# Optimization experiments

Measured on AMD Instinct MI355X. Metric: run time of the kernel, lower is better.

## Reference

```python
import jax, jax.numpy as jnp
import numpy as np

B, CIN, COUT, K, H, W, WDIM = 16, 512, 512, 3, 64, 64, 512


def setup_inputs() -> dict:
    key = jax.random.key(0)
    k1, k2, k3, k4 = jax.random.split(key, 4)
    x = jax.random.normal(k1, (B, CIN, H, W), dtype=jnp.float32)
    w = jax.random.normal(k2, (B, WDIM), dtype=jnp.float32)
    # Equalized-LR init: init_std = 1/lrmul = 1.0 -> unit normal weights
    conv_w = jax.random.normal(k3, (K, K, CIN, COUT), dtype=jnp.float32)
    mod_w = jax.random.normal(k4, (WDIM, CIN), dtype=jnp.float32)
    mod_b = jnp.zeros((CIN,), dtype=jnp.float32)
    return {"x": x, "w": w, "conv_w": conv_w, "mod_w": mod_w, "mod_b": mod_b}


def reference(x, w, conv_w, mod_w, mod_b):
    # runtime coefficients (gain=1, lrmul=1): he_std = gain/sqrt(fan_in)
    coef_conv = np.float32(1.0 / np.sqrt(K * K * CIN))
    coef_mod = np.float32(1.0 / np.sqrt(WDIM))

    # style modulation: Dense + Bias + 1.0  -> [B, CIN]
    style = w @ (coef_mod * mod_w) + mod_b + 1.0

    # per-sample modulated weight [B, K, K, CIN, COUT]
    weight = (coef_conv * conv_w)[None] * style[:, None, None, :, None]

    # demodulate: rsqrt of sum of squares over (K, K, CIN) per output channel
    d = jax.lax.rsqrt(jnp.sum(jnp.square(weight), axis=(1, 2, 3)) + 1e-8)  # [B, COUT]
    weight = weight * d[:, None, None, None, :]

    # grouped conv via batch->channel-group reshape (StyleGAN2 trick)
    wg = jnp.transpose(weight, (1, 2, 3, 0, 4)).reshape(K, K, CIN, B * COUT)
    xg = x.reshape(1, B * CIN, H, W)
    y = jax.lax.conv_general_dilated(
        xg, wg, window_strides=(1, 1), padding="SAME",
        dimension_numbers=("NCHW", "HWIO", "NCHW"),
        feature_group_count=B,
    )
    return y.reshape(B, COUT, H, W)
```

## Files before the change

### kernel.cpp

```cpp
#include <hip/hip_runtime.h>
#include <hip/hip_bf16.h>

#define NB    16
#define CIN   512
#define COUT  512
#define HH    64
#define WW    64
#define HWSZ  4096
#define WDIMN 512

typedef __attribute__((ext_vector_type(8))) short bf16x8;
typedef __attribute__((ext_vector_type(4))) float f32x4;

__device__ __forceinline__ unsigned short f2bf(float f) {
    unsigned int u = __float_as_uint(f);
    unsigned int lsb = (u >> 16) & 1u;
    u += 0x7fffu + lsb;
    return (unsigned short)(u >> 16);
}

__device__ __forceinline__ void gload_lds16(const void* g, void* l) {
    __builtin_amdgcn_global_load_lds(
        (const __attribute__((address_space(1))) unsigned char*)g,
        (__attribute__((address_space(3))) unsigned char*)l,
        16, 0, 0);
}

__global__ void k_style(const float* __restrict__ w, const float* __restrict__ mod_w,
                        const float* __restrict__ mod_b, float* __restrict__ style) {
    const int b = blockIdx.x, t = threadIdx.x;
    __shared__ float wl[WDIMN];
    wl[t] = w[b * WDIMN + t];
    wl[t + 256] = w[b * WDIMN + t + 256];
    __syncthreads();
    float a0 = 0.f, a1 = 0.f;
    const int c0 = t, c1 = t + 256;
    for (int j = 0; j < WDIMN; ++j) {
        const float wj = wl[j];
        a0 += wj * mod_w[j * CIN + c0];
        a1 += wj * mod_w[j * CIN + c1];
    }
    const float coef = 0.044194173824159216f;
    style[b * CIN + c0] = coef * a0 + mod_b[c0] + 1.0f;
    style[b * CIN + c1] = coef * a1 + mod_b[c1] + 1.0f;
}

__global__ void k_s2(const float* __restrict__ cw, float* __restrict__ s2) {
    const int i = blockIdx.x * 256 + threadIdx.x;
    float a = 0.f;
#pragma unroll
    for (int tap = 0; tap < 9; ++tap) {
        const float v = cw[tap * (CIN * COUT) + i];
        a += v * v;
    }
    s2[i] = a;
}

__global__ void k_demod(const float* __restrict__ style, const float* __restrict__ s2,
                        float* __restrict__ dd) {
    const int b = blockIdx.x, t = threadIdx.x;
    __shared__ float st2[CIN];
    {
        const float s0 = style[b * CIN + t], s1 = style[b * CIN + t + 256];
        st2[t] = s0 * s0;
        st2[t + 256] = s1 * s1;
    }
    __syncthreads();
    float a0 = 0.f, a1 = 0.f;
    for (int ci = 0; ci < CIN; ++ci) {
        const float sv = st2[ci];
        a0 += sv * s2[ci * COUT + t];
        a1 += sv * s2[ci * COUT + t + 256];
    }
    const float c2 = 1.0f / 4608.0f;
    dd[b * COUT + t] = rsqrtf(c2 * a0 + 1e-8f);
    dd[b * COUT + t + 256] = rsqrtf(c2 * a1 + 1e-8f);
}

__global__ void k_wmod(const float* __restrict__ cw, const float* __restrict__ style,
                       const float* __restrict__ dd, unsigned short* __restrict__ wmod,
                       int b_start, int gcount) {
    const int tap = blockIdx.x;
    const int co0 = blockIdx.y * 64;
    const int ci0 = blockIdx.z * 128;
    const int t = threadIdx.x;

    __shared__ float tile[128][65];
    {
        const int j = t & 63, isub = t >> 6;
        for (int i = isub; i < 128; i += 4)
            tile[i][j] = cw[(size_t)tap * CIN * COUT + (size_t)(ci0 + i) * COUT + co0 + j];
    }
    __syncthreads();

    const float coef = 0.014731391274719736f;
    const int cp = t & 63;
    const int rsub = t >> 6;
    const int totrows = gcount * 64;
    for (int g = rsub; g < totrows; g += 4) {
        const int bbl = g >> 6;
        const int co_r = g & 63;
        const int bg = b_start + bbl;
        const float dv = dd[bg * COUT + co0 + co_r] * coef;
        const float s0 = style[bg * CIN + ci0 + 2 * cp];
        const float s1 = style[bg * CIN + ci0 + 2 * cp + 1];
        const float v0 = tile[2 * cp][co_r] * s0 * dv;
        const float v1 = tile[2 * cp + 1][co_r] * s1 * dv;
        const unsigned int pk = (unsigned int)f2bf(v0) | ((unsigned int)f2bf(v1) << 16);
        *(unsigned int*)&wmod[((size_t)(bbl * 9 + tap) * COUT + co0 + co_r) * CIN + ci0 + 2 * cp] = pk;
    }
}

__global__ void k_xt(const float* __restrict__ x, unsigned short* __restrict__ xT, int b_start) {
    const int bbl = blockIdx.x;
    const int b = b_start + bbl;
    const int hw0 = blockIdx.y * 64;
    const int ci0 = blockIdx.z * 64;
    const int t = threadIdx.x;

    __shared__ float tile[64][65];
    {
        const int j = t & 63, isub = t >> 6;
        for (int i = isub; i < 64; i += 4)
            tile[i][j] = x[((size_t)b * CIN + ci0 + i) * HWSZ + hw0 + j];
    }
    __syncthreads();

    const int cp = t & 31;
    const int rs = t >> 5;
    for (int r = rs; r < 64; r += 8) {
        const float v0 = tile[2 * cp][r];
        const float v1 = tile[2 * cp + 1][r];
        const unsigned int pk = (unsigned int)f2bf(v0) | ((unsigned int)f2bf(v1) << 16);
        *(unsigned int*)&xT[((size_t)bbl * HWSZ + hw0 + r) * CIN + ci0 + 2 * cp] = pk;
    }
}

__global__ __launch_bounds__(256, 2)
void k_conv(const unsigned short* __restrict__ xT, const unsigned short* __restrict__ wmod,
            float* __restrict__ out, int b_start) {
    const int st = blockIdx.x;
    const int ct = blockIdx.y;
    const int bbl = blockIdx.z;
    const int b = b_start + bbl;
    const int r0 = st * 2;
    const int co0 = ct * 128;

    const int t = threadIdx.x;
    const int lane = t & 63;
    const int wid = t >> 6;
    const int wrow = wid >> 1;
    const int wcol = wid & 1;

    __shared__ __align__(16) unsigned char smem[4 * 66 * 128 + 2 * 128 * 128];
    unsigned char* Xs = smem;
    unsigned char* As = smem + 4 * 66 * 128;

    const f32x4 fzero = {0.f, 0.f, 0.f, 0.f};

    if (t < 64) {
        const int s = t >> 3;
        const int row = s >> 1, col = (s & 1) ? 65 : 0;
        *(f32x4*)(Xs + (row * 66 + col) * 128 + (t & 7) * 16) = fzero;
    }
    if (r0 == 0) {
        for (int idx = t; idx < 66 * 8; idx += 256)
            *(f32x4*)(Xs + (idx >> 3) * 128 + (idx & 7) * 16) = fzero;
    }
    if (r0 == 62) {
        for (int idx = t; idx < 66 * 8; idx += 256)
            *(f32x4*)(Xs + (3 * 66 + (idx >> 3)) * 128 + (idx & 7) * 16) = fzero;
    }

    f32x4 acc[4][4];
#pragma unroll
    for (int i = 0; i < 4; ++i)
#pragma unroll
        for (int j = 0; j < 4; ++j) acc[i][j] = fzero;

    const size_t xTbase = (size_t)bbl * HWSZ * CIN;

    auto stageA = [&](int tap, int bsel, int ci0) {
        const unsigned short* gb = wmod + ((size_t)(bbl * 9 + tap) * COUT + co0) * CIN + ci0;
        unsigned char* dbase = As + bsel * 16384;
#pragma unroll
        for (int i = 0; i < 4; ++i) {
            const int la = wid + 4 * i;
            const int row = la * 8 + (lane >> 3);
            const int kb = ((lane & 7) * 16) ^ ((row & 7) << 4);
            gload_lds16((const unsigned char*)(gb + (size_t)row * CIN) + kb,
                        dbase + la * 1024);
        }
    };

    int buf = 0;
    for (int cc = 0; cc < 8; ++cc) {
        const int ci0 = cc * 64;

#pragma unroll
        for (int i = 0; i < 8; ++i) {
            const int li = wid + 4 * i;
            const int row = li >> 3;
            const int c0 = 1 + (li & 7) * 8;
            const int ih = r0 - 1 + row;
            if (ih >= 0 && ih < HH) {
                const int col = c0 + (lane >> 3);
                const int pxidx = row * 66 + col;
                const int kb = ((lane & 7) * 16) ^ ((pxidx & 7) << 4);
                const int iw = col - 1;
                gload_lds16((const unsigned char*)(xT + xTbase + (size_t)(ih * WW + iw) * CIN + ci0) + kb,
                            Xs + (row * 66 + c0) * 128);
            }
        }

        stageA(0, buf, ci0);
        __syncthreads();

        for (int tap = 0; tap < 9; ++tap) {
            if (tap < 8) stageA(tap + 1, buf ^ 1, ci0);
            const int dh = tap / 3 - 1, dw = tap % 3 - 1;
            const unsigned char* Ab = As + buf * 16384;
#pragma unroll
            for (int k32 = 0; k32 < 2; ++k32) {
                bf16x8 af[4], bfv[4];
#pragma unroll
                for (int ma = 0; ma < 4; ++ma) {
                    const int co_r = wrow * 64 + ma * 16 + (lane & 15);
                    const int kb = (k32 * 64 + (lane >> 4) * 16) ^ ((co_r & 7) << 4);
                    af[ma] = *(const bf16x8*)(Ab + co_r * 128 + kb);
                }
#pragma unroll
                for (int nb = 0; nb < 4; ++nb) {
                    const int px = wcol * 64 + nb * 16 + (lane & 15);
                    const int trow = (px >> 6) + 1 + dh;
                    const int tcol = (px & 63) + 1 + dw;
                    const int pxidx = trow * 66 + tcol;
                    const int kb = (k32 * 64 + (lane >> 4) * 16) ^ ((pxidx & 7) << 4);
                    bfv[nb] = *(const bf16x8*)(Xs + pxidx * 128 + kb);
                }
#pragma unroll
                for (int ma = 0; ma < 4; ++ma)
#pragma unroll
                    for (int nb = 0; nb < 4; ++nb)
                        acc[ma][nb] = __builtin_amdgcn_mfma_f32_16x16x32_bf16(
                            af[ma], bfv[nb], acc[ma][nb], 0, 0, 0);
            }
            __syncthreads();
            buf ^= 1;
        }
    }

#pragma unroll
    for (int ma = 0; ma < 4; ++ma) {
        const int co = co0 + wrow * 64 + ma * 16 + ((lane >> 4) << 2);
#pragma unroll
        for (int nb = 0; nb < 4; ++nb) {
            const int px = wcol * 64 + nb * 16 + (lane & 15);
            const int oh = r0 + (px >> 6);
            const int ow = px & 63;
            float* o = out + (((size_t)b * COUT + co) * HH + oh) * WW + ow;
#pragma unroll
            for (int jj = 0; jj < 4; ++jj) o[(size_t)jj * HWSZ] = acc[ma][nb][jj];
        }
    }
}

extern "C" void kernel_launch(void* const* d_in, const int* in_sizes, int n_in,
                              void* d_out, int out_size, void* d_ws, size_t ws_size,
                              hipStream_t stream) {
    (void)in_sizes; (void)n_in; (void)out_size;
    const float* x     = (const float*)d_in[0];
    const float* w     = (const float*)d_in[1];
    const float* convw = (const float*)d_in[2];
    const float* mod_w = (const float*)d_in[3];
    const float* mod_b = (const float*)d_in[4];
    float* out = (float*)d_out;

    unsigned char* ws = (unsigned char*)d_ws;
    const size_t OFF_STYLE = 0;
    const size_t OFF_S2 = 32768;
    const size_t OFF_D = OFF_S2 + 1048576;
    const size_t OFF_BIG = OFF_D + 32768;
    const size_t PER_B_W = (size_t)9 * COUT * CIN * 2;
    const size_t PER_B_X = (size_t)HWSZ * CIN * 2;
    const size_t PER_B = PER_B_W + PER_B_X;

    if (ws_size < OFF_BIG + PER_B) return;
    const size_t avail = ws_size - OFF_BIG;
    const int G = (avail >= 16 * PER_B) ? 16 : (avail >= 4 * PER_B ? 4 : 1);

    float* style = (float*)(ws + OFF_STYLE);
    float* s2    = (float*)(ws + OFF_S2);
    float* dd    = (float*)(ws + OFF_D);
    unsigned short* wmod = (unsigned short*)(ws + OFF_BIG);
    unsigned short* xT   = (unsigned short*)(ws + OFF_BIG + (size_t)G * PER_B_W);

    k_style<<<dim3(16), dim3(256), 0, stream>>>(w, mod_w, mod_b, style);
    k_s2<<<dim3(1024), dim3(256), 0, stream>>>(convw, s2);
    k_demod<<<dim3(16), dim3(256), 0, stream>>>(style, s2, dd);

    for (int b0 = 0; b0 < NB; b0 += G) {
        k_wmod<<<dim3(9, 8, 4), dim3(256), 0, stream>>>(convw, style, dd, wmod, b0, G);
        k_xt<<<dim3(G, 64, 8), dim3(256), 0, stream>>>(x, xT, b0);
        k_conv<<<dim3(32, 4, G), dim3(256), 0, stream>>>(xT, wmod, out, b0);
    }
}
```

Before: 461.0 us.

## Enlarge conv tile to 256 output channels with 8 waves and a deeper LDS pipeline

Each conv block now has 512 threads and covers 256 output channels, so every staged X tile is reused by twice as many channels. The X tile is double-buffered across input-channel chunks, and the weight tile is prefetched two taps ahead using explicit vmcnt/lgkmcnt waits and raw barriers instead of __syncthreads. All fragments are loaded into registers before the MFMA burst, which runs at raised priority. The aim is to hide global-to-LDS latency and cut synchronisation cost, at the price of more LDS (about 130KB per block) and more register pressure.

New measurement: 866.8 us. 88.0% more time.

```diff
diff --git a/kernel.cpp b/kernel.cpp
--- a/kernel.cpp
+++ b/kernel.cpp
@@ -136,7 +136,10 @@
     }
 }
 
-__global__ __launch_bounds__(256, 2)
+#define A_STRIDE 32768
+#define X_OFF    65536
+#define X_STRIDE 33792
+__global__ __launch_bounds__(512, 2)
 void k_conv(const unsigned short* __restrict__ xT, const unsigned short* __restrict__ wmod,
             float* __restrict__ out, int b_start) {
     const int st = blockIdx.x;
@@ -144,7 +147,7 @@
     const int bbl = blockIdx.z;
     const int b = b_start + bbl;
     const int r0 = st * 2;
-    const int co0 = ct * 128;
+    const int co0 = ct * 256;
 
     const int t = threadIdx.x;
     const int lane = t & 63;
@@ -152,54 +155,49 @@
     const int wrow = wid >> 1;
     const int wcol = wid & 1;
 
-    __shared__ __align__(16) unsigned char smem[4 * 66 * 128 + 2 * 128 * 128];
-    unsigned char* Xs = smem;
-    unsigned char* As = smem + 4 * 66 * 128;
+    __shared__ __align__(16) unsigned char smem[2 * A_STRIDE + 2 * X_STRIDE];
 
     const f32x4 fzero = {0.f, 0.f, 0.f, 0.f};
 
-    if (t < 64) {
+    if (t < 128) {
         const int s = t >> 3;
-        const int row = s >> 1, col = (s & 1) ? 65 : 0;
-        *(f32x4*)(Xs + (row * 66 + col) * 128 + (t & 7) * 16) = fzero;
+        unsigned char* Xb = smem + X_OFF + ((s >> 3) & 1) * X_STRIDE;
+        const int row = (s >> 1) & 3, col = (s & 1) ? 65 : 0;
+        *(f32x4*)(Xb + (row * 66 + col) * 128 + (t & 7) * 16) = fzero;
     }
     if (r0 == 0) {
-        for (int idx = t; idx < 66 * 8; idx += 256)
-            *(f32x4*)(Xs + (idx >> 3) * 128 + (idx & 7) * 16) = fzero;
+        for (int idx = t; idx < 2 * 66 * 8; idx += 512) {
+            unsigned char* Xb = smem + X_OFF + (idx >= 66 * 8 ? X_STRIDE : 0);
+            const int k = idx % (66 * 8);
+            *(f32x4*)(Xb + (k >> 3) * 128 + (k & 7) * 16) = fzero;
+        }
     }
     if (r0 == 62) {
-        for (int idx = t; idx < 66 * 8; idx += 256)
-            *(f32x4*)(Xs + (3 * 66 + (idx >> 3)) * 128 + (idx & 7) * 16) = fzero;
-    }
-
-    f32x4 acc[4][4];
-#pragma unroll
-    for (int i = 0; i < 4; ++i)
-#pragma unroll
-        for (int j = 0; j < 4; ++j) acc[i][j] = fzero;
+        for (int idx = t; idx < 2 * 66 * 8; idx += 512) {
+            unsigned char* Xb = smem + X_OFF + (idx >= 66 * 8 ? X_STRIDE : 0);
+            const int k = idx % (66 * 8);
+            *(f32x4*)(Xb + (3 * 66 + (k >> 3)) * 128 + (k & 7) * 16) = fzero;
+        }
+    }
 
     const size_t xTbase = (size_t)bbl * HWSZ * CIN;
 
-    auto stageA = [&](int tap, int bsel, int ci0) {
-        const unsigned short* gb = wmod + ((size_t)(bbl * 9 + tap) * COUT + co0) * CIN + ci0;
-        unsigned char* dbase = As + bsel * 16384;
+    auto stageA = [&](int cc2, int tap2, unsigned char* dst) {
+        const unsigned short* gb = wmod + ((size_t)(bbl * 9 + tap2) * COUT + co0) * CIN + cc2 * 64;
 #pragma unroll
         for (int i = 0; i < 4; ++i) {
-            const int la = wid + 4 * i;
-            const int row = la * 8 + (lane >> 3);
+            const int j = wid + 8 * i;
+            const int row = j * 8 + (lane >> 3);
             const int kb = ((lane & 7) * 16) ^ ((row & 7) << 4);
             gload_lds16((const unsigned char*)(gb + (size_t)row * CIN) + kb,
-                        dbase + la * 1024);
+                        dst + j * 1024);
         }
     };
-
-    int buf = 0;
-    for (int cc = 0; cc < 8; ++cc) {
-        const int ci0 = cc * 64;
-
-#pragma unroll
-        for (int i = 0; i < 8; ++i) {
-            const int li = wid + 4 * i;
+    auto stageX = [&](int ccn, unsigned char* dst) {
+        const int ci0 = ccn * 64;
+#pragma unroll
+        for (int i = 0; i < 4; ++i) {
+            const int li = wid + 8 * i;
             const int row = li >> 3;
             const int c0 = 1 + (li & 7) * 8;
             const int ih = r0 - 1 + row;
@@ -207,46 +205,78 @@
                 const int col = c0 + (lane >> 3);
                 const int pxidx = row * 66 + col;
                 const int kb = ((lane & 7) * 16) ^ ((pxidx & 7) << 4);
-                const int iw = col - 1;
-                gload_lds16((const unsigned char*)(xT + xTbase + (size_t)(ih * WW + iw) * CIN + ci0) + kb,
-                            Xs + (row * 66 + c0) * 128);
+                gload_lds16((const unsigned char*)(xT + xTbase + (size_t)(ih * WW + col - 1) * CIN + ci0) + kb,
+                            dst + (row * 66 + c0) * 128);
             }
         }
-
-        stageA(0, buf, ci0);
-        __syncthreads();
-
+    };
+
+    f32x4 acc[4][4];
+#pragma unroll
+    for (int i = 0; i < 4; ++i)
+#pragma unroll
+        for (int j = 0; j < 4; ++j) acc[i][j] = fzero;
+
+    stageX(0, smem + X_OFF);
+    stageA(0, 0, smem);
+    stageA(0, 1, smem + A_STRIDE);
+    asm volatile("s_waitcnt lgkmcnt(0)" ::: "memory");
+
+    for (int cc = 0; cc < 8; ++cc) {
+        unsigned char* Xcur = smem + X_OFF + (cc & 1) * X_STRIDE;
+        unsigned char* Xnxt = smem + X_OFF + ((cc & 1) ^ 1) * X_STRIDE;
+#pragma unroll
         for (int tap = 0; tap < 9; ++tap) {
-            if (tap < 8) stageA(tap + 1, buf ^ 1, ci0);
+            unsigned char* Rcur = smem + ((cc + tap) & 1) * A_STRIDE;
+
+            asm volatile("s_waitcnt vmcnt(4)" ::: "memory");
+            __builtin_amdgcn_s_barrier();
+            __builtin_amdgcn_sched_barrier(0);
+
+            bf16x8 af[2][4], bfv[2][4];
             const int dh = tap / 3 - 1, dw = tap % 3 - 1;
-            const unsigned char* Ab = As + buf * 16384;
 #pragma unroll
             for (int k32 = 0; k32 < 2; ++k32) {
-                bf16x8 af[4], bfv[4];
 #pragma unroll
                 for (int ma = 0; ma < 4; ++ma) {
                     const int co_r = wrow * 64 + ma * 16 + (lane & 15);
                     const int kb = (k32 * 64 + (lane >> 4) * 16) ^ ((co_r & 7) << 4);
-                    af[ma] = *(const bf16x8*)(Ab + co_r * 128 + kb);
+                    af[k32][ma] = *(const bf16x8*)(Rcur + co_r * 128 + kb);
                 }
 #pragma unroll
                 for (int nb = 0; nb < 4; ++nb) {
                     const int px = wcol * 64 + nb * 16 + (lane & 15);
-                    const int trow = (px >> 6) + 1 + dh;
+                    const int trow = wcol + 1 + dh;
                     const int tcol = (px & 63) + 1 + dw;
                     const int pxidx = trow * 66 + tcol;
                     const int kb = (k32 * 64 + (lane >> 4) * 16) ^ ((pxidx & 7) << 4);
-                    bfv[nb] = *(const bf16x8*)(Xs + pxidx * 128 + kb);
+                    bfv[k32][nb] = *(const bf16x8*)(Xcur + pxidx * 128 + kb);
                 }
+            }
+            asm volatile("s_waitcnt lgkmcnt(0)" ::: "memory");
+            __builtin_amdgcn_sched_barrier(0);
+            __builtin_amdgcn_s_barrier();
+            __builtin_amdgcn_sched_barrier(0);
+
+            if (tap == 0 && cc < 7) stageX(cc + 1, Xnxt);
+            {
+                int cc2, tap2;
+                if (tap < 7) { cc2 = cc; tap2 = tap + 2; }
+                else { cc2 = cc + 1; tap2 = tap - 7; if (cc2 > 7) { cc2 = 7; tap2 = 8; } }
+                stageA(cc2, tap2, Rcur);
+            }
+            __builtin_amdgcn_sched_barrier(0);
+
+            __builtin_amdgcn_s_setprio(1);
+#pragma unroll
+            for (int k32 = 0; k32 < 2; ++k32)
 #pragma unroll
                 for (int ma = 0; ma < 4; ++ma)
 #pragma unroll
                     for (int nb = 0; nb < 4; ++nb)
                         acc[ma][nb] = __builtin_amdgcn_mfma_f32_16x16x32_bf16(
-                            af[ma], bfv[nb], acc[ma][nb], 0, 0, 0);
-            }
-            __syncthreads();
-            buf ^= 1;
+                            af[k32][ma], bfv[k32][nb], acc[ma][nb], 0, 0, 0);
+            __builtin_amdgcn_s_setprio(0);
         }
     }
 
@@ -256,7 +286,7 @@
 #pragma unroll
         for (int nb = 0; nb < 4; ++nb) {
             const int px = wcol * 64 + nb * 16 + (lane & 15);
-            const int oh = r0 + (px >> 6);
+            const int oh = r0 + wcol;
             const int ow = px & 63;
             float* o = out + (((size_t)b * COUT + co) * HH + oh) * WW + ow;
 #pragma unroll
@@ -302,6 +332,6 @@
     for (int b0 = 0; b0 < NB; b0 += G) {
         k_wmod<<<dim3(9, 8, 4), dim3(256), 0, stream>>>(convw, style, dd, wmod, b0, G);
         k_xt<<<dim3(G, 64, 8), dim3(256), 0, stream>>>(x, xT, b0);
-        k_conv<<<dim3(32, 4, G), dim3(256), 0, stream>>>(xT, wmod, out, b0);
-    }
-}
+        k_conv<<<dim3(32, 2, G), dim3(512), 0, stream>>>(xT, wmod, out, b0);
+    }
+}
```
